# Optimization experiments

Hardware: AMD Instinct MI355X
Metric: run time of the kernel (lower is better)

The kernel has to match this reference:

```python
import jax, jax.numpy as jnp
import numpy as np

X = 2048      # hidden units per layer
Z = 4         # number of hidden layers
IN = 512      # input_dim
OUT = 256     # output_dim
B = 64        # batch
T = 128       # time steps
KEEP = 0.7    # Bernoulli keep prob y
RES = [0, 0, 1, 2]  # residual_in (first two unused by the branch structure)
NFUN = 5      # number of candidate transfer functions


def setup_inputs() -> dict:
    key = jax.random.key(0)
    ks = jax.random.split(key, 12)
    f32 = jnp.float32
    x = jax.random.normal(ks[0], (B, T, IN), f32)
    W_in = jax.random.normal(ks[1], (X, IN), f32) * jax.random.bernoulli(ks[2], KEEP, (X, IN)).astype(f32)
    b_in = jax.random.normal(ks[3], (X,), f32)
    W_h = jax.random.normal(ks[4], (Z, X, 2 * X), f32)
    # lateral inhibition block: hidden layer 1, second-half columns, zero diagonal
    lat = jax.random.normal(ks[5], (X, X), f32) * (1.0 - jnp.eye(X, dtype=f32))
    W_h = W_h.at[1, :, X:].set(lat)
    W_h = W_h * jax.random.bernoulli(ks[6], KEEP, (Z, X, 2 * X)).astype(f32)
    b_h = jax.random.normal(ks[7], (Z, X), f32)
    W_out = jax.random.normal(ks[8], (OUT, X), f32) * jax.random.bernoulli(ks[9], KEEP, (OUT, X)).astype(f32)
    b_out = jax.random.normal(ks[10], (OUT,), f32)
    act_ids = jax.random.randint(ks[11], (Z + 1, X), 0, NFUN)
    out_act_ids = jax.random.randint(jax.random.fold_in(key, 99), (OUT,), 0, NFUN)
    return dict(x=x, W_in=W_in, b_in=b_in, W_h=W_h, b_h=b_h,
                W_out=W_out, b_out=b_out, act_ids=act_ids, out_act_ids=out_act_ids)


def _rand_act(h, ids):
    # per-column random nonlinearity: ids [D] in {relu, sigmoid, tanh, leaky_relu(0.1), selu}
    stk = jnp.stack([
        jax.nn.relu(h),
        jax.nn.sigmoid(h),
        jnp.tanh(h),
        jnp.where(h >= 0, h, 0.1 * h),
        jax.nn.selu(h),
    ], axis=0)  # [5, B, D]
    oh = jax.nn.one_hot(ids, NFUN, dtype=h.dtype)  # [D, 5]
    return jnp.einsum('fbd,df->bd', stk, oh)


def _l2norm(v, eps=1e-12):
    # torch F.normalize along dim=1
    return v / jnp.maximum(jnp.linalg.norm(v, axis=1, keepdims=True), eps)


def reference(x, W_in, b_in, W_h, b_h, W_out, b_out, act_ids, out_act_ids):
    batch = x.shape[0]

    def step(carry, xt):
        bp, li = carry  # backprojection state, lateral inhibition state
        h0 = _rand_act(xt @ W_in.T + b_in, act_ids[0])
        h1 = _rand_act(jnp.concatenate([h0, bp], axis=-1) @ W_h[0].T + b_h[0], act_ids[1])
        h2 = _rand_act(jnp.concatenate([h1, li], axis=-1) @ W_h[1].T + b_h[1], act_ids[2])
        li_new = _l2norm(h2)
        outs = [h0, h1, h2]
        for i in range(2, Z):
            hin = jnp.concatenate([outs[i], outs[RES[i]]], axis=-1)
            outs.append(_rand_act(hin @ W_h[i].T + b_h[i], act_ids[i + 1]))
        bp_new = _l2norm(outs[-1])
        yt = _rand_act(outs[-1] @ W_out.T + b_out, out_act_ids)
        return (bp_new, li_new), yt

    init = (jnp.zeros((batch, X), x.dtype), jnp.zeros((batch, X), x.dtype))
    _, ys = jax.lax.scan(step, init, jnp.swapaxes(x, 0, 1))  # scan over time
    return jnp.swapaxes(ys, 0, 1)  # [B, T, OUT]
```

## Files before the change

kernel.cpp:

```cpp
#include <hip/hip_runtime.h>
#include <stdint.h>


typedef __bf16 bf16;
typedef __attribute__((ext_vector_type(8))) __bf16 bf16x8;
typedef __attribute__((ext_vector_type(4))) float f32x4;

#define BATCH 64
#define TSTEPS 128
#define INDIM 512
#define XDIM 2048
#define OUTDIM 256

__device__ __forceinline__ float apply_act(float h, int id) {
  switch (id) {
    case 0: return fmaxf(h, 0.0f);
    case 1: return 1.0f / (1.0f + __expf(-h));
    case 2: return tanhf(h);
    case 3: return h >= 0.0f ? h : 0.1f * h;
    default: {
      const float sc = 1.0507009873554805f;
      const float al = 1.6732632423543772f;
      return h > 0.0f ? sc * h : sc * al * (__expf(h) - 1.0f);
    }
  }
}

template <int KPW, bool HAS_A2, bool SCALE_A2, bool EMIT_SS, int MODE>
__global__ __launch_bounds__(256) void step_gemm(
    const bf16* __restrict__ A1, const bf16* __restrict__ A2,
    const bf16* __restrict__ W, const float* __restrict__ bias,
    const int* __restrict__ acts, const float* __restrict__ ss_in,
    float* __restrict__ ss_out, bf16* __restrict__ outb,
    float* __restrict__ outf, int KTOT, int N, int t) {
  const int tid = threadIdx.x;
  const int lane = tid & 63;
  const int w = tid >> 6;
  const int l15 = lane & 15;
  const int kb8 = (lane >> 4) * 8;
  const int nblk = blockIdx.x * 16;
  const int mrow = blockIdx.y * 32;

  const bf16* As;
  int koff, wk;
  if (HAS_A2) {
    As = (w >= 2) ? A2 : A1;
    koff = (w & 1) * KPW;
    wk = (w >= 2 ? 2048 : 0) + koff;
  } else {
    As = A1;
    koff = w * KPW;
    wk = koff;
  }

  const bf16* ap0 = As + (size_t)(mrow + l15) * 2048 + koff + kb8;
  const bf16* ap1 = ap0 + 16 * 2048;
  const bf16* bpw = W + (size_t)(nblk + l15) * KTOT + wk + kb8;

  f32x4 acc0 = {0.f, 0.f, 0.f, 0.f};
  f32x4 acc1 = {0.f, 0.f, 0.f, 0.f};
#pragma unroll 4
  for (int k = 0; k < KPW; k += 32) {
    bf16x8 a0 = *(const bf16x8*)(ap0 + k);
    bf16x8 a1 = *(const bf16x8*)(ap1 + k);
    bf16x8 b  = *(const bf16x8*)(bpw + k);
    acc0 = __builtin_amdgcn_mfma_f32_16x16x32_bf16(a0, b, acc0, 0, 0, 0);
    acc1 = __builtin_amdgcn_mfma_f32_16x16x32_bf16(a1, b, acc1, 0, 0, 0);
  }

  __shared__ float red[4][32][17];
  const int q4 = lane >> 4;
#pragma unroll
  for (int r = 0; r < 4; r++) red[w][q4 * 4 + r][l15] = acc0[r];
#pragma unroll
  for (int r = 0; r < 4; r++) red[w][16 + q4 * 4 + r][l15] = acc1[r];
  __syncthreads();

  const int row = tid >> 3;
  const int c0 = (tid & 7) * 2;
  const int rg = mrow + row;

  float scale = 1.0f;
  if (SCALE_A2) {
    float nrm = sqrtf(ss_in[rg]);
    scale = 1.0f / fmaxf(nrm, 1e-12f);
  }

  float v[2];
#pragma unroll
  for (int j = 0; j < 2; j++) {
    int c = c0 + j;
    float lo = red[0][row][c] + red[1][row][c];
    float hi = red[2][row][c] + red[3][row][c];
    float pre = SCALE_A2 ? (lo + scale * hi) : (lo + hi);
    int n = nblk + c;
    pre += bias[n];
    v[j] = apply_act(pre, acts[n]);
  }

  if (EMIT_SS) {
    float ss = v[0] * v[0] + v[1] * v[1];
    ss += __shfl_xor(ss, 1);
    ss += __shfl_xor(ss, 2);
    ss += __shfl_xor(ss, 4);
    if ((tid & 7) == 0) atomicAdd(ss_out + rg, ss);
  }

  if (MODE == 0) {
    union { bf16 b2[2]; uint32_t u; } pk;
    pk.b2[0] = (bf16)v[0];
    pk.b2[1] = (bf16)v[1];
    *(uint32_t*)(outb + (size_t)rg * N + nblk + c0) = pk.u;
  } else {
    *(float2*)(outf + ((size_t)rg * TSTEPS + t) * OUTDIM + nblk + c0) =
        make_float2(v[0], v[1]);
  }
}

__global__ __launch_bounds__(256) void h0_gemm(
    const bf16* __restrict__ A, const bf16* __restrict__ W,
    const float* __restrict__ bias, const int* __restrict__ acts,
    bf16* __restrict__ outp) {
  const int tid = threadIdx.x;
  const int lane = tid & 63;
  const int wv = tid >> 6;
  const int wm = (wv & 1) * 32;
  const int wn = (wv >> 1) * 64;
  const int nblk = blockIdx.x * 128;
  const int mblk = blockIdx.y * 64;
  const int l15 = lane & 15;
  const int kb8 = (lane >> 4) * 8;

  f32x4 acc[2][4];
  const f32x4 zero = {0.f, 0.f, 0.f, 0.f};
#pragma unroll
  for (int i = 0; i < 2; i++)
#pragma unroll
    for (int j = 0; j < 4; j++) acc[i][j] = zero;

  for (int kt = 0; kt < INDIM; kt += 32) {
    bf16x8 a[2], b[4];
#pragma unroll
    for (int mt = 0; mt < 2; mt++) {
      int m = mblk + wm + mt * 16 + l15;
      a[mt] = *(const bf16x8*)(A + (size_t)m * INDIM + kt + kb8);
    }
#pragma unroll
    for (int nt = 0; nt < 4; nt++) {
      int n = nblk + wn + nt * 16 + l15;
      b[nt] = *(const bf16x8*)(W + (size_t)n * INDIM + kt + kb8);
    }
#pragma unroll
    for (int mt = 0; mt < 2; mt++)
#pragma unroll
      for (int nt = 0; nt < 4; nt++)
        acc[mt][nt] = __builtin_amdgcn_mfma_f32_16x16x32_bf16(a[mt], b[nt], acc[mt][nt], 0, 0, 0);
  }

#pragma unroll
  for (int mt = 0; mt < 2; mt++) {
#pragma unroll
    for (int nt = 0; nt < 4; nt++) {
      int n = nblk + wn + nt * 16 + l15;
      float bv = bias[n];
      int aid = acts[n];
#pragma unroll
      for (int rr = 0; rr < 4; rr++) {
        int m = wm + mt * 16 + (lane >> 4) * 4 + rr;
        float v = apply_act(acc[mt][nt][rr] + bv, aid);
        int rowg = mblk + m;
        int bb = rowg >> 7;
        int tt = rowg & 127;
        outp[((size_t)tt * BATCH + bb) * XDIM + n] = (bf16)v;
      }
    }
  }
}

__global__ __launch_bounds__(256) void cvt_bf16(
    const float* __restrict__ in, bf16* __restrict__ out, int n4) {
  int i = blockIdx.x * 256 + threadIdx.x;
  if (i < n4) {
    float4 v = ((const float4*)in)[i];
    union { bf16 b[4]; unsigned long long u; } pk;
    pk.b[0] = (bf16)v.x;
    pk.b[1] = (bf16)v.y;
    pk.b[2] = (bf16)v.z;
    pk.b[3] = (bf16)v.w;
    ((unsigned long long*)out)[i] = pk.u;
  }
}

__global__ __launch_bounds__(256) void zero32(uint32_t* __restrict__ p, int n) {
  int i = blockIdx.x * 256 + threadIdx.x;
  if (i < n) p[i] = 0u;
}

extern "C" void kernel_launch(void* const* d_in, const int* in_sizes, int n_in,
                              void* d_out, int out_size, void* d_ws, size_t ws_size,
                              hipStream_t stream) {
  const float* x     = (const float*)d_in[0];
  const float* W_in  = (const float*)d_in[1];
  const float* b_in  = (const float*)d_in[2];
  const float* W_h   = (const float*)d_in[3];
  const float* b_h   = (const float*)d_in[4];
  const float* W_out = (const float*)d_in[5];
  const float* b_out = (const float*)d_in[6];
  const int* act_ids = (const int*)d_in[7];
  const int* out_act = (const int*)d_in[8];
  float* out = (float*)d_out;

  char* w = (char*)d_ws;
  bf16* xbf   = (bf16*)w; w += (size_t)BATCH * TSTEPS * INDIM * 2;
  bf16* winb  = (bf16*)w; w += (size_t)XDIM * INDIM * 2;
  bf16* whb   = (bf16*)w; w += (size_t)4 * XDIM * (2 * XDIM) * 2;
  bf16* woutb = (bf16*)w; w += (size_t)OUTDIM * XDIM * 2;
  bf16* h0    = (bf16*)w; w += (size_t)TSTEPS * BATCH * XDIM * 2;
  bf16* h1    = (bf16*)w; w += (size_t)BATCH * XDIM * 2;
  bf16* h3    = (bf16*)w; w += (size_t)BATCH * XDIM * 2;
  char* zstart = w;
  bf16* h2a   = (bf16*)w; w += (size_t)BATCH * XDIM * 2;
  bf16* h2b   = (bf16*)w; w += (size_t)BATCH * XDIM * 2;
  bf16* h4    = (bf16*)w; w += (size_t)BATCH * XDIM * 2;
  float* ss_li = (float*)w; w += (size_t)(TSTEPS + 1) * BATCH * 4;
  float* ss_bp = (float*)w; w += (size_t)(TSTEPS + 1) * BATCH * 4;
  int zero_u32 = (int)((w - zstart) / 4);

  cvt_bf16<<<4096, 256, 0, stream>>>(x, xbf, (BATCH * TSTEPS * INDIM) / 4);
  cvt_bf16<<<1024, 256, 0, stream>>>(W_in, winb, (XDIM * INDIM) / 4);
  cvt_bf16<<<32768, 256, 0, stream>>>(W_h, whb, (4 * XDIM * 2 * XDIM) / 4);
  cvt_bf16<<<512, 256, 0, stream>>>(W_out, woutb, (OUTDIM * XDIM) / 4);

  zero32<<<(zero_u32 + 255) / 256, 256, 0, stream>>>((uint32_t*)zstart, zero_u32);

  h0_gemm<<<dim3(16, 128), 256, 0, stream>>>(xbf, winb, b_in, act_ids, h0);

  const size_t wstride = (size_t)XDIM * 2 * XDIM;
  for (int t = 0; t < TSTEPS; t++) {
    const bf16* h0t = h0 + (size_t)t * BATCH * XDIM;
    bf16* h2_new = (t & 1) ? h2b : h2a;
    bf16* h2_old = (t & 1) ? h2a : h2b;

    step_gemm<1024, true, true, false, 0><<<dim3(128, 2), 256, 0, stream>>>(
        h0t, h4, whb + 0 * wstride, b_h + 0 * XDIM, act_ids + 1 * XDIM,
        ss_bp + t * BATCH, nullptr, h1, nullptr, 4096, XDIM, t);
    step_gemm<1024, true, true, true, 0><<<dim3(128, 2), 256, 0, stream>>>(
        h1, h2_old, whb + 1 * wstride, b_h + 1 * XDIM, act_ids + 2 * XDIM,
        ss_li + t * BATCH, ss_li + (t + 1) * BATCH, h2_new, nullptr, 4096, XDIM, t);
    step_gemm<1024, true, false, false, 0><<<dim3(128, 2), 256, 0, stream>>>(
        h2_new, h1, whb + 2 * wstride, b_h + 2 * XDIM, act_ids + 3 * XDIM,
        nullptr, nullptr, h3, nullptr, 4096, XDIM, t);
    step_gemm<1024, true, false, true, 0><<<dim3(128, 2), 256, 0, stream>>>(
        h3, h2_new, whb + 3 * wstride, b_h + 3 * XDIM, act_ids + 4 * XDIM,
        nullptr, ss_bp + (t + 1) * BATCH, h4, nullptr, 4096, XDIM, t);
    step_gemm<512, false, false, false, 1><<<dim3(16, 2), 256, 0, stream>>>(
        h4, nullptr, woutb, b_out, out_act,
        nullptr, nullptr, nullptr, out, 2048, OUTDIM, t);
  }
}
```

Baseline: 10.21 ms.

## Replace per-timestep kernel launches with a persistent cooperative kernel using grid barriers

The 640 small per-step GEMM launches are replaced by one cooperative persistent kernel of 256 workgroups. The kernel steps through time with a hand-written atomic grid barrier between layer phases. The output projection for step t-1 runs on 32 of the workgroups alongside the first layer of step t, which removes its separate phase. This targets launch overhead and inter-kernel gaps, but adds spin-barrier latency and needs all 256 workgroups to be co-resident.

Result: slower. 19.66 ms (+92.6%).

```diff
diff --git a/kernel.cpp b/kernel.cpp
--- a/kernel.cpp
+++ b/kernel.cpp
@@ -11,6 +11,7 @@
 #define INDIM 512
 #define XDIM 2048
 #define OUTDIM 256
+#define NWG 256
 
 __device__ __forceinline__ float apply_act(float h, int id) {
   switch (id) {
@@ -26,41 +27,52 @@
   }
 }
 
-template <int KPW, bool HAS_A2, bool SCALE_A2, bool EMIT_SS, int MODE>
-__global__ __launch_bounds__(256) void step_gemm(
+__device__ __forceinline__ void gbar(uint32_t* cnt, uint32_t* ep, uint32_t target) {
+  __syncthreads();
+  if (threadIdx.x == 0) {
+    __threadfence();
+    uint32_t prev = __hip_atomic_fetch_add(cnt, 1u, __ATOMIC_ACQ_REL, __HIP_MEMORY_SCOPE_AGENT);
+    if (prev == NWG - 1) {
+      __hip_atomic_store(cnt, 0u, __ATOMIC_RELAXED, __HIP_MEMORY_SCOPE_AGENT);
+      __hip_atomic_fetch_add(ep, 1u, __ATOMIC_RELEASE, __HIP_MEMORY_SCOPE_AGENT);
+    } else {
+      while (__hip_atomic_load(ep, __ATOMIC_RELAXED, __HIP_MEMORY_SCOPE_AGENT) < target) {
+        __builtin_amdgcn_s_sleep(2);
+      }
+    }
+    __threadfence();
+  }
+  __syncthreads();
+}
+
+template <bool SCALE_A2, bool EMIT_SS>
+__device__ __forceinline__ void hphase(
+    int n_tile, int m_half,
     const bf16* __restrict__ A1, const bf16* __restrict__ A2,
     const bf16* __restrict__ W, const float* __restrict__ bias,
     const int* __restrict__ acts, const float* __restrict__ ss_in,
     float* __restrict__ ss_out, bf16* __restrict__ outb,
-    float* __restrict__ outf, int KTOT, int N, int t) {
+    float red[4][32][17]) {
   const int tid = threadIdx.x;
   const int lane = tid & 63;
   const int w = tid >> 6;
   const int l15 = lane & 15;
   const int kb8 = (lane >> 4) * 8;
-  const int nblk = blockIdx.x * 16;
-  const int mrow = blockIdx.y * 32;
-
-  const bf16* As;
-  int koff, wk;
-  if (HAS_A2) {
-    As = (w >= 2) ? A2 : A1;
-    koff = (w & 1) * KPW;
-    wk = (w >= 2 ? 2048 : 0) + koff;
-  } else {
-    As = A1;
-    koff = w * KPW;
-    wk = koff;
-  }
+  const int nblk = n_tile * 16;
+  const int mrow = m_half * 32;
+
+  const bf16* As = (w >= 2) ? A2 : A1;
+  const int koff = (w & 1) * 1024;
+  const int wk = (w >= 2 ? 2048 : 0) + koff;
 
   const bf16* ap0 = As + (size_t)(mrow + l15) * 2048 + koff + kb8;
   const bf16* ap1 = ap0 + 16 * 2048;
-  const bf16* bpw = W + (size_t)(nblk + l15) * KTOT + wk + kb8;
+  const bf16* bpw = W + (size_t)(nblk + l15) * 4096 + wk + kb8;
 
   f32x4 acc0 = {0.f, 0.f, 0.f, 0.f};
   f32x4 acc1 = {0.f, 0.f, 0.f, 0.f};
 #pragma unroll 4
-  for (int k = 0; k < KPW; k += 32) {
+  for (int k = 0; k < 1024; k += 32) {
     bf16x8 a0 = *(const bf16x8*)(ap0 + k);
     bf16x8 a1 = *(const bf16x8*)(ap1 + k);
     bf16x8 b  = *(const bf16x8*)(bpw + k);
@@ -68,7 +80,6 @@
     acc1 = __builtin_amdgcn_mfma_f32_16x16x32_bf16(a1, b, acc1, 0, 0, 0);
   }
 
-  __shared__ float red[4][32][17];
   const int q4 = lane >> 4;
 #pragma unroll
   for (int r = 0; r < 4; r++) red[w][q4 * 4 + r][l15] = acc0[r];
@@ -79,12 +90,8 @@
   const int row = tid >> 3;
   const int c0 = (tid & 7) * 2;
   const int rg = mrow + row;
-
   float scale = 1.0f;
-  if (SCALE_A2) {
-    float nrm = sqrtf(ss_in[rg]);
-    scale = 1.0f / fmaxf(nrm, 1e-12f);
-  }
+  if (SCALE_A2) scale = 1.0f / fmaxf(sqrtf(ss_in[rg]), 1e-12f);
 
   float v[2];
 #pragma unroll
@@ -92,12 +99,9 @@
     int c = c0 + j;
     float lo = red[0][row][c] + red[1][row][c];
     float hi = red[2][row][c] + red[3][row][c];
-    float pre = SCALE_A2 ? (lo + scale * hi) : (lo + hi);
-    int n = nblk + c;
-    pre += bias[n];
-    v[j] = apply_act(pre, acts[n]);
-  }
-
+    float pre = (SCALE_A2 ? (lo + scale * hi) : (lo + hi)) + bias[nblk + c];
+    v[j] = apply_act(pre, acts[nblk + c]);
+  }
   if (EMIT_SS) {
     float ss = v[0] * v[0] + v[1] * v[1];
     ss += __shfl_xor(ss, 1);
@@ -105,16 +109,113 @@
     ss += __shfl_xor(ss, 4);
     if ((tid & 7) == 0) atomicAdd(ss_out + rg, ss);
   }
-
-  if (MODE == 0) {
-    union { bf16 b2[2]; uint32_t u; } pk;
-    pk.b2[0] = (bf16)v[0];
-    pk.b2[1] = (bf16)v[1];
-    *(uint32_t*)(outb + (size_t)rg * N + nblk + c0) = pk.u;
-  } else {
-    *(float2*)(outf + ((size_t)rg * TSTEPS + t) * OUTDIM + nblk + c0) =
-        make_float2(v[0], v[1]);
-  }
+  union { bf16 b2[2]; uint32_t u; } pk;
+  pk.b2[0] = (bf16)v[0];
+  pk.b2[1] = (bf16)v[1];
+  *(uint32_t*)(outb + (size_t)rg * XDIM + nblk + c0) = pk.u;
+}
+
+__device__ void yphase(int idx, const bf16* __restrict__ h4,
+                       const bf16* __restrict__ Wout,
+                       const float* __restrict__ bout,
+                       const int* __restrict__ oact,
+                       float* __restrict__ out, int t,
+                       float red[4][32][17]) {
+  __syncthreads();
+  const int tid = threadIdx.x;
+  const int lane = tid & 63;
+  const int w = tid >> 6;
+  const int l15 = lane & 15;
+  const int kb8 = (lane >> 4) * 8;
+  const int nblk = (idx & 15) * 16;
+  const int mrow = (idx >> 4) * 32;
+  const int koff = w * 512;
+
+  const bf16* ap0 = h4 + (size_t)(mrow + l15) * 2048 + koff + kb8;
+  const bf16* ap1 = ap0 + 16 * 2048;
+  const bf16* bpw = Wout + (size_t)(nblk + l15) * 2048 + koff + kb8;
+
+  f32x4 acc0 = {0.f, 0.f, 0.f, 0.f};
+  f32x4 acc1 = {0.f, 0.f, 0.f, 0.f};
+#pragma unroll 4
+  for (int k = 0; k < 512; k += 32) {
+    bf16x8 a0 = *(const bf16x8*)(ap0 + k);
+    bf16x8 a1 = *(const bf16x8*)(ap1 + k);
+    bf16x8 b  = *(const bf16x8*)(bpw + k);
+    acc0 = __builtin_amdgcn_mfma_f32_16x16x32_bf16(a0, b, acc0, 0, 0, 0);
+    acc1 = __builtin_amdgcn_mfma_f32_16x16x32_bf16(a1, b, acc1, 0, 0, 0);
+  }
+  const int q4 = lane >> 4;
+#pragma unroll
+  for (int r = 0; r < 4; r++) red[w][q4 * 4 + r][l15] = acc0[r];
+#pragma unroll
+  for (int r = 0; r < 4; r++) red[w][16 + q4 * 4 + r][l15] = acc1[r];
+  __syncthreads();
+
+  const int row = tid >> 3;
+  const int c0 = (tid & 7) * 2;
+  const int rg = mrow + row;
+  float v[2];
+#pragma unroll
+  for (int j = 0; j < 2; j++) {
+    int c = c0 + j;
+    float pre = red[0][row][c] + red[1][row][c] + red[2][row][c] +
+                red[3][row][c] + bout[nblk + c];
+    v[j] = apply_act(pre, oact[nblk + c]);
+  }
+  *(float2*)(out + ((size_t)rg * TSTEPS + t) * OUTDIM + nblk + c0) =
+      make_float2(v[0], v[1]);
+}
+
+struct Params {
+  const bf16* h0;
+  const bf16* whb;
+  const float* b_h;
+  const int* act_ids;
+  const bf16* woutb;
+  const float* b_out;
+  const int* out_act;
+  bf16 *h1, *h2a, *h2b, *h3, *h4;
+  float *ss_li, *ss_bp, *out;
+  uint32_t *cnt, *ep;
+};
+
+__global__ __launch_bounds__(256) void bnn_persistent(Params p) {
+  __shared__ float red[4][32][17];
+  const int wg = blockIdx.x;
+  const int n_tile = wg & 127;
+  const int m_half = wg >> 7;
+  const size_t wstr = (size_t)XDIM * 2 * XDIM;
+  uint32_t bt = 0;
+
+  for (int t = 0; t < TSTEPS; t++) {
+    const bf16* h0t = p.h0 + (size_t)t * BATCH * XDIM;
+    bf16* h2n = (t & 1) ? p.h2b : p.h2a;
+    bf16* h2o = (t & 1) ? p.h2a : p.h2b;
+
+    hphase<true, false>(n_tile, m_half, h0t, p.h4, p.whb, p.b_h,
+                        p.act_ids + XDIM, p.ss_bp + t * BATCH, nullptr, p.h1, red);
+    if (wg >= 224 && t > 0)
+      yphase(wg - 224, p.h4, p.woutb, p.b_out, p.out_act, p.out, t - 1, red);
+    gbar(p.cnt, p.ep, ++bt);
+
+    hphase<true, true>(n_tile, m_half, p.h1, h2o, p.whb + wstr, p.b_h + XDIM,
+                       p.act_ids + 2 * XDIM, p.ss_li + t * BATCH,
+                       p.ss_li + (t + 1) * BATCH, h2n, red);
+    gbar(p.cnt, p.ep, ++bt);
+
+    hphase<false, false>(n_tile, m_half, h2n, p.h1, p.whb + 2 * wstr,
+                         p.b_h + 2 * XDIM, p.act_ids + 3 * XDIM,
+                         nullptr, nullptr, p.h3, red);
+    gbar(p.cnt, p.ep, ++bt);
+
+    hphase<false, true>(n_tile, m_half, p.h3, h2n, p.whb + 3 * wstr,
+                        p.b_h + 3 * XDIM, p.act_ids + 4 * XDIM, nullptr,
+                        p.ss_bp + (t + 1) * BATCH, p.h4, red);
+    gbar(p.cnt, p.ep, ++bt);
+  }
+  if (wg >= 224)
+    yphase(wg - 224, p.h4, p.woutb, p.b_out, p.out_act, p.out, TSTEPS - 1, red);
 }
 
 __global__ __launch_bounds__(256) void h0_gemm(
@@ -224,37 +325,24 @@
   bf16* h4    = (bf16*)w; w += (size_t)BATCH * XDIM * 2;
   float* ss_li = (float*)w; w += (size_t)(TSTEPS + 1) * BATCH * 4;
   float* ss_bp = (float*)w; w += (size_t)(TSTEPS + 1) * BATCH * 4;
+  uint32_t* barv = (uint32_t*)w; w += 256;
   int zero_u32 = (int)((w - zstart) / 4);
 
   cvt_bf16<<<4096, 256, 0, stream>>>(x, xbf, (BATCH * TSTEPS * INDIM) / 4);
   cvt_bf16<<<1024, 256, 0, stream>>>(W_in, winb, (XDIM * INDIM) / 4);
   cvt_bf16<<<32768, 256, 0, stream>>>(W_h, whb, (4 * XDIM * 2 * XDIM) / 4);
   cvt_bf16<<<512, 256, 0, stream>>>(W_out, woutb, (OUTDIM * XDIM) / 4);
-
   zero32<<<(zero_u32 + 255) / 256, 256, 0, stream>>>((uint32_t*)zstart, zero_u32);
-
   h0_gemm<<<dim3(16, 128), 256, 0, stream>>>(xbf, winb, b_in, act_ids, h0);
 
-  const size_t wstride = (size_t)XDIM * 2 * XDIM;
-  for (int t = 0; t < TSTEPS; t++) {
-    const bf16* h0t = h0 + (size_t)t * BATCH * XDIM;
-    bf16* h2_new = (t & 1) ? h2b : h2a;
-    bf16* h2_old = (t & 1) ? h2a : h2b;
-
-    step_gemm<1024, true, true, false, 0><<<dim3(128, 2), 256, 0, stream>>>(
-        h0t, h4, whb + 0 * wstride, b_h + 0 * XDIM, act_ids + 1 * XDIM,
-        ss_bp + t * BATCH, nullptr, h1, nullptr, 4096, XDIM, t);
-    step_gemm<1024, true, true, true, 0><<<dim3(128, 2), 256, 0, stream>>>(
-        h1, h2_old, whb + 1 * wstride, b_h + 1 * XDIM, act_ids + 2 * XDIM,
-        ss_li + t * BATCH, ss_li + (t + 1) * BATCH, h2_new, nullptr, 4096, XDIM, t);
-    step_gemm<1024, true, false, false, 0><<<dim3(128, 2), 256, 0, stream>>>(
-        h2_new, h1, whb + 2 * wstride, b_h + 2 * XDIM, act_ids + 3 * XDIM,
-        nullptr, nullptr, h3, nullptr, 4096, XDIM, t);
-    step_gemm<1024, true, false, true, 0><<<dim3(128, 2), 256, 0, stream>>>(
-        h3, h2_new, whb + 3 * wstride, b_h + 3 * XDIM, act_ids + 4 * XDIM,
-        nullptr, ss_bp + (t + 1) * BATCH, h4, nullptr, 4096, XDIM, t);
-    step_gemm<512, false, false, false, 1><<<dim3(16, 2), 256, 0, stream>>>(
-        h4, nullptr, woutb, b_out, out_act,
-        nullptr, nullptr, nullptr, out, 2048, OUTDIM, t);
-  }
-}
+  Params P;
+  P.h0 = h0; P.whb = whb; P.b_h = b_h; P.act_ids = act_ids;
+  P.woutb = woutb; P.b_out = b_out; P.out_act = out_act;
+  P.h1 = h1; P.h2a = h2a; P.h2b = h2b; P.h3 = h3; P.h4 = h4;
+  P.ss_li = ss_li; P.ss_bp = ss_bp; P.out = out;
+  P.cnt = barv; P.ep = barv + 1;
+
+  void* kargs[] = {&P};
+  hipLaunchCooperativeKernel((const void*)bnn_persistent, dim3(NWG), dim3(256),
+                             kargs, 0, stream);
+}
```

## Split K across eight waves and batch output GEMM over all timesteps

Applied to the files above, without the earlier changes.

Each recurrent step GEMM now uses 512-thread blocks with eight waves, each covering a 512-wide K slice, instead of four waves over 1024-wide slices. This gives more loads in flight per block on the latency-bound weight stream. The per-step output projection is removed from the time loop. Each step's h4 is written into a rotating slot, reusing the h0 buffer of already-consumed timesteps, and a single batched GEMM over all timesteps computes the outputs at the end. This cuts one launch per step and turns many tiny GEMMs into one larger one, at the cost of more intricate buffer aliasing.

After: 8.867 ms. 13.1% less time.

```diff
diff --git a/kernel.cpp b/kernel.cpp
--- a/kernel.cpp
+++ b/kernel.cpp
@@ -11,6 +11,7 @@
 #define INDIM 512
 #define XDIM 2048
 #define OUTDIM 256
+#define SLOTE ((size_t)BATCH * XDIM)
 
 __device__ __forceinline__ float apply_act(float h, int id) {
   switch (id) {
@@ -26,13 +27,12 @@
   }
 }
 
-template <int KPW, bool HAS_A2, bool SCALE_A2, bool EMIT_SS, int MODE>
-__global__ __launch_bounds__(256) void step_gemm(
+template <bool SCALE_A2, bool EMIT_SS>
+__global__ __launch_bounds__(512, 2) void step_gemm8(
     const bf16* __restrict__ A1, const bf16* __restrict__ A2,
     const bf16* __restrict__ W, const float* __restrict__ bias,
     const int* __restrict__ acts, const float* __restrict__ ss_in,
-    float* __restrict__ ss_out, bf16* __restrict__ outb,
-    float* __restrict__ outf, int KTOT, int N, int t) {
+    float* __restrict__ ss_out, bf16* __restrict__ outb) {
   const int tid = threadIdx.x;
   const int lane = tid & 63;
   const int w = tid >> 6;
@@ -41,26 +41,18 @@
   const int nblk = blockIdx.x * 16;
   const int mrow = blockIdx.y * 32;
 
-  const bf16* As;
-  int koff, wk;
-  if (HAS_A2) {
-    As = (w >= 2) ? A2 : A1;
-    koff = (w & 1) * KPW;
-    wk = (w >= 2 ? 2048 : 0) + koff;
-  } else {
-    As = A1;
-    koff = w * KPW;
-    wk = koff;
-  }
+  const bf16* As = (w >= 4) ? A2 : A1;
+  const int koff = (w & 3) * 512;
+  const int wk = w * 512;
 
   const bf16* ap0 = As + (size_t)(mrow + l15) * 2048 + koff + kb8;
   const bf16* ap1 = ap0 + 16 * 2048;
-  const bf16* bpw = W + (size_t)(nblk + l15) * KTOT + wk + kb8;
+  const bf16* bpw = W + (size_t)(nblk + l15) * 4096 + wk + kb8;
 
   f32x4 acc0 = {0.f, 0.f, 0.f, 0.f};
   f32x4 acc1 = {0.f, 0.f, 0.f, 0.f};
-#pragma unroll 4
-  for (int k = 0; k < KPW; k += 32) {
+#pragma unroll
+  for (int k = 0; k < 512; k += 32) {
     bf16x8 a0 = *(const bf16x8*)(ap0 + k);
     bf16x8 a1 = *(const bf16x8*)(ap1 + k);
     bf16x8 b  = *(const bf16x8*)(bpw + k);
@@ -68,7 +60,7 @@
     acc1 = __builtin_amdgcn_mfma_f32_16x16x32_bf16(a1, b, acc1, 0, 0, 0);
   }
 
-  __shared__ float red[4][32][17];
+  __shared__ float red[8][32][17];
   const int q4 = lane >> 4;
 #pragma unroll
   for (int r = 0; r < 4; r++) red[w][q4 * 4 + r][l15] = acc0[r];
@@ -76,44 +68,34 @@
   for (int r = 0; r < 4; r++) red[w][16 + q4 * 4 + r][l15] = acc1[r];
   __syncthreads();
 
-  const int row = tid >> 3;
-  const int c0 = (tid & 7) * 2;
-  const int rg = mrow + row;
-
-  float scale = 1.0f;
-  if (SCALE_A2) {
-    float nrm = sqrtf(ss_in[rg]);
-    scale = 1.0f / fmaxf(nrm, 1e-12f);
-  }
-
-  float v[2];
-#pragma unroll
-  for (int j = 0; j < 2; j++) {
-    int c = c0 + j;
-    float lo = red[0][row][c] + red[1][row][c];
-    float hi = red[2][row][c] + red[3][row][c];
-    float pre = SCALE_A2 ? (lo + scale * hi) : (lo + hi);
-    int n = nblk + c;
-    pre += bias[n];
-    v[j] = apply_act(pre, acts[n]);
-  }
-
-  if (EMIT_SS) {
-    float ss = v[0] * v[0] + v[1] * v[1];
-    ss += __shfl_xor(ss, 1);
-    ss += __shfl_xor(ss, 2);
-    ss += __shfl_xor(ss, 4);
-    if ((tid & 7) == 0) atomicAdd(ss_out + rg, ss);
-  }
-
-  if (MODE == 0) {
+  if (tid < 256) {
+    const int row = tid >> 3;
+    const int c0 = (tid & 7) * 2;
+    const int rg = mrow + row;
+
+    float scale = 1.0f;
+    if (SCALE_A2) scale = 1.0f / fmaxf(sqrtf(ss_in[rg]), 1e-12f);
+
+    float v[2];
+#pragma unroll
+    for (int j = 0; j < 2; j++) {
+      int c = c0 + j;
+      float lo = red[0][row][c] + red[1][row][c] + red[2][row][c] + red[3][row][c];
+      float hi = red[4][row][c] + red[5][row][c] + red[6][row][c] + red[7][row][c];
+      float pre = (SCALE_A2 ? (lo + scale * hi) : (lo + hi)) + bias[nblk + c];
+      v[j] = apply_act(pre, acts[nblk + c]);
+    }
+    if (EMIT_SS) {
+      float ss = v[0] * v[0] + v[1] * v[1];
+      ss += __shfl_xor(ss, 1);
+      ss += __shfl_xor(ss, 2);
+      ss += __shfl_xor(ss, 4);
+      if ((tid & 7) == 0) atomicAdd(ss_out + rg, ss);
+    }
     union { bf16 b2[2]; uint32_t u; } pk;
     pk.b2[0] = (bf16)v[0];
     pk.b2[1] = (bf16)v[1];
-    *(uint32_t*)(outb + (size_t)rg * N + nblk + c0) = pk.u;
-  } else {
-    *(float2*)(outf + ((size_t)rg * TSTEPS + t) * OUTDIM + nblk + c0) =
-        make_float2(v[0], v[1]);
+    *(uint32_t*)(outb + (size_t)rg * XDIM + nblk + c0) = pk.u;
   }
 }
 
@@ -177,6 +159,66 @@
   }
 }
 
+__global__ __launch_bounds__(256) void ybat_gemm(
+    const bf16* __restrict__ extra, const bf16* __restrict__ h0,
+    const bf16* __restrict__ Wout, const float* __restrict__ bout,
+    const int* __restrict__ oact, float* __restrict__ out) {
+  const int t = blockIdx.y;
+  const int s = t + 1;
+  const bf16* A = (s < 2) ? (extra + (size_t)s * SLOTE)
+                          : (h0 + (size_t)(s - 2) * SLOTE);
+  const int tid = threadIdx.x;
+  const int lane = tid & 63;
+  const int wv = tid >> 6;
+  const int wm = (wv & 1) * 32;
+  const int wn = (wv >> 1) * 64;
+  const int nblk = blockIdx.x * 128;
+  const int l15 = lane & 15;
+  const int kb8 = (lane >> 4) * 8;
+
+  f32x4 acc[2][4];
+  const f32x4 zero = {0.f, 0.f, 0.f, 0.f};
+#pragma unroll
+  for (int i = 0; i < 2; i++)
+#pragma unroll
+    for (int j = 0; j < 4; j++) acc[i][j] = zero;
+
+  for (int kt = 0; kt < XDIM; kt += 32) {
+    bf16x8 a[2], b[4];
+#pragma unroll
+    for (int mt = 0; mt < 2; mt++) {
+      int m = wm + mt * 16 + l15;
+      a[mt] = *(const bf16x8*)(A + (size_t)m * XDIM + kt + kb8);
+    }
+#pragma unroll
+    for (int nt = 0; nt < 4; nt++) {
+      int n = nblk + wn + nt * 16 + l15;
+      b[nt] = *(const bf16x8*)(Wout + (size_t)n * XDIM + kt + kb8);
+    }
+#pragma unroll
+    for (int mt = 0; mt < 2; mt++)
+#pragma unroll
+      for (int nt = 0; nt < 4; nt++)
+        acc[mt][nt] = __builtin_amdgcn_mfma_f32_16x16x32_bf16(a[mt], b[nt], acc[mt][nt], 0, 0, 0);
+  }
+
+#pragma unroll
+  for (int mt = 0; mt < 2; mt++) {
+#pragma unroll
+    for (int nt = 0; nt < 4; nt++) {
+      int n = nblk + wn + nt * 16 + l15;
+      float bv = bout[n];
+      int aid = oact[n];
+#pragma unroll
+      for (int rr = 0; rr < 4; rr++) {
+        int b = wm + mt * 16 + (lane >> 4) * 4 + rr;
+        float v = apply_act(acc[mt][nt][rr] + bv, aid);
+        out[((size_t)b * TSTEPS + t) * OUTDIM + n] = v;
+      }
+    }
+  }
+}
+
 __global__ __launch_bounds__(256) void cvt_bf16(
     const float* __restrict__ in, bf16* __restrict__ out, int n4) {
   int i = blockIdx.x * 256 + threadIdx.x;
@@ -215,13 +257,13 @@
   bf16* winb  = (bf16*)w; w += (size_t)XDIM * INDIM * 2;
   bf16* whb   = (bf16*)w; w += (size_t)4 * XDIM * (2 * XDIM) * 2;
   bf16* woutb = (bf16*)w; w += (size_t)OUTDIM * XDIM * 2;
-  bf16* h0    = (bf16*)w; w += (size_t)TSTEPS * BATCH * XDIM * 2;
-  bf16* h1    = (bf16*)w; w += (size_t)BATCH * XDIM * 2;
-  bf16* h3    = (bf16*)w; w += (size_t)BATCH * XDIM * 2;
+  bf16* h0    = (bf16*)w; w += (size_t)TSTEPS * SLOTE * 2;
+  bf16* h1    = (bf16*)w; w += SLOTE * 2;
+  bf16* h3    = (bf16*)w; w += SLOTE * 2;
   char* zstart = w;
-  bf16* h2a   = (bf16*)w; w += (size_t)BATCH * XDIM * 2;
-  bf16* h2b   = (bf16*)w; w += (size_t)BATCH * XDIM * 2;
-  bf16* h4    = (bf16*)w; w += (size_t)BATCH * XDIM * 2;
+  bf16* extra = (bf16*)w; w += 2 * SLOTE * 2;
+  bf16* h2a   = (bf16*)w; w += SLOTE * 2;
+  bf16* h2b   = (bf16*)w; w += SLOTE * 2;
   float* ss_li = (float*)w; w += (size_t)(TSTEPS + 1) * BATCH * 4;
   float* ss_bp = (float*)w; w += (size_t)(TSTEPS + 1) * BATCH * 4;
   int zero_u32 = (int)((w - zstart) / 4);
@@ -230,31 +272,32 @@
   cvt_bf16<<<1024, 256, 0, stream>>>(W_in, winb, (XDIM * INDIM) / 4);
   cvt_bf16<<<32768, 256, 0, stream>>>(W_h, whb, (4 * XDIM * 2 * XDIM) / 4);
   cvt_bf16<<<512, 256, 0, stream>>>(W_out, woutb, (OUTDIM * XDIM) / 4);
-
   zero32<<<(zero_u32 + 255) / 256, 256, 0, stream>>>((uint32_t*)zstart, zero_u32);
-
   h0_gemm<<<dim3(16, 128), 256, 0, stream>>>(xbf, winb, b_in, act_ids, h0);
 
-  const size_t wstride = (size_t)XDIM * 2 * XDIM;
+  auto slotp = [&](int s) -> bf16* {
+    return (s < 2) ? (extra + (size_t)s * SLOTE) : (h0 + (size_t)(s - 2) * SLOTE);
+  };
+
+  const size_t wstr = (size_t)XDIM * 2 * XDIM;
   for (int t = 0; t < TSTEPS; t++) {
-    const bf16* h0t = h0 + (size_t)t * BATCH * XDIM;
-    bf16* h2_new = (t & 1) ? h2b : h2a;
-    bf16* h2_old = (t & 1) ? h2a : h2b;
-
-    step_gemm<1024, true, true, false, 0><<<dim3(128, 2), 256, 0, stream>>>(
-        h0t, h4, whb + 0 * wstride, b_h + 0 * XDIM, act_ids + 1 * XDIM,
-        ss_bp + t * BATCH, nullptr, h1, nullptr, 4096, XDIM, t);
-    step_gemm<1024, true, true, true, 0><<<dim3(128, 2), 256, 0, stream>>>(
-        h1, h2_old, whb + 1 * wstride, b_h + 1 * XDIM, act_ids + 2 * XDIM,
-        ss_li + t * BATCH, ss_li + (t + 1) * BATCH, h2_new, nullptr, 4096, XDIM, t);
-    step_gemm<1024, true, false, false, 0><<<dim3(128, 2), 256, 0, stream>>>(
-        h2_new, h1, whb + 2 * wstride, b_h + 2 * XDIM, act_ids + 3 * XDIM,
-        nullptr, nullptr, h3, nullptr, 4096, XDIM, t);
-    step_gemm<1024, true, false, true, 0><<<dim3(128, 2), 256, 0, stream>>>(
-        h3, h2_new, whb + 3 * wstride, b_h + 3 * XDIM, act_ids + 4 * XDIM,
-        nullptr, ss_bp + (t + 1) * BATCH, h4, nullptr, 4096, XDIM, t);
-    step_gemm<512, false, false, false, 1><<<dim3(16, 2), 256, 0, stream>>>(
-        h4, nullptr, woutb, b_out, out_act,
-        nullptr, nullptr, nullptr, out, 2048, OUTDIM, t);
-  }
-}
+    bf16* h2n = (t & 1) ? h2b : h2a;
+    bf16* h2o = (t & 1) ? h2a : h2b;
+
+    step_gemm8<true, false><<<dim3(128, 2), 512, 0, stream>>>(
+        h0 + (size_t)t * SLOTE, slotp(t), whb, b_h, act_ids + XDIM,
+        ss_bp + t * BATCH, nullptr, h1);
+    step_gemm8<true, true><<<dim3(128, 2), 512, 0, stream>>>(
+        h1, h2o, whb + wstr, b_h + XDIM, act_ids + 2 * XDIM,
+        ss_li + t * BATCH, ss_li + (t + 1) * BATCH, h2n);
+    step_gemm8<false, false><<<dim3(128, 2), 512, 0, stream>>>(
+        h2n, h1, whb + 2 * wstr, b_h + 2 * XDIM, act_ids + 3 * XDIM,
+        nullptr, nullptr, h3);
+    step_gemm8<false, true><<<dim3(128, 2), 512, 0, stream>>>(
+        h3, h2n, whb + 3 * wstr, b_h + 3 * XDIM, act_ids + 4 * XDIM,
+        nullptr, ss_bp + (t + 1) * BATCH, slotp(t + 1));
+  }
+
+  ybat_gemm<<<dim3(2, TSTEPS), 256, 0, stream>>>(
+      extra, h0, woutb, b_out, out_act, out);
+}
```
